# Kernel optimization log

Measured on AMD Instinct MI355X. Metric: run time of the kernel, lower is better.

Reference implementation:

```python
import math
import jax, jax.numpy as jnp
import numpy as np

C = 1024  # n_embd
B, T = 4, 2048
H = 4 * C  # mlp hidden
EPS = 1e-5


def setup_inputs() -> dict:
    key = jax.random.key(0)
    ks = jax.random.split(key, 8)
    s = 0.02
    return {
        "x": jax.random.normal(ks[0], (B, T, C), jnp.float32),
        "ln1_g": jnp.ones((C,), jnp.float32),
        "ln1_b": jnp.zeros((C,), jnp.float32),
        "w_attn": jax.random.normal(ks[1], (C, 3 * C), jnp.float32) * s,
        "b_attn": jnp.zeros((3 * C,), jnp.float32),
        "w_proj": jax.random.normal(ks[2], (C, C), jnp.float32) * s,
        "b_proj": jnp.zeros((C,), jnp.float32),
        "ln2_g": jnp.ones((C,), jnp.float32),
        "ln2_b": jnp.zeros((C,), jnp.float32),
        "w_fc": jax.random.normal(ks[3], (C, H), jnp.float32) * s,
        "b_fc": jnp.zeros((H,), jnp.float32),
        "w_mlp_proj": jax.random.normal(ks[4], (H, C), jnp.float32) * s,
        "b_mlp_proj": jnp.zeros((C,), jnp.float32),
    }


def _layernorm(x, g, b):
    mu = jnp.mean(x, axis=-1, keepdims=True)
    var = jnp.mean(jnp.square(x - mu), axis=-1, keepdims=True)
    return (x - mu) * jax.lax.rsqrt(var + EPS) * g + b


def _new_gelu(x):
    c = math.sqrt(2.0 / math.pi)
    return 0.5 * x * (1.0 + jnp.tanh(c * (x + 0.044715 * x * x * x)))


def reference(x, ln1_g, ln1_b, w_attn, b_attn, w_proj, b_proj,
              ln2_g, ln2_b, w_fc, b_fc, w_mlp_proj, b_mlp_proj):
    # --- attention sublayer (single-head, full-dim, no causal mask) ---
    h = _layernorm(x, ln1_g, ln1_b)
    qkv = h @ w_attn + b_attn              # [B,T,3C]
    q, k, v = jnp.split(qkv, 3, axis=-1)   # each [B,T,C]
    scale = 1.0 / math.sqrt(C)
    att = jnp.einsum("btc,bsc->bts", q, k) * scale  # [B,T,T]
    att = jax.nn.softmax(att, axis=-1)
    y = jnp.einsum("bts,bsc->btc", att, v)
    y = y @ w_proj + b_proj
    x = x + y
    # --- MLP sublayer ---
    h2 = _layernorm(x, ln2_g, ln2_b)
    m = _new_gelu(h2 @ w_fc + b_fc) @ w_mlp_proj + b_mlp_proj
    return x + m
```

## Files before the change

kernel.cpp:

```cpp
#include <hip/hip_runtime.h>

typedef __bf16 bf16;
typedef bf16 bf16x8 __attribute__((ext_vector_type(8)));
typedef bf16 bf16x4 __attribute__((ext_vector_type(4)));
typedef float f32x4 __attribute__((ext_vector_type(4)));

#define C_DIM 1024
#define T_DIM 2048
#define B_DIM 4
#define H_DIM 4096

__device__ inline void gld_lds16(const bf16* g, bf16* l) {
    __builtin_amdgcn_global_load_lds(
        (const __attribute__((address_space(1))) unsigned int*)g,
        (__attribute__((address_space(3))) unsigned int*)l,
        16, 0, 0);
}

__device__ inline float fast_gelu(float u) {
    float k2 = 1.5957691216057308f * u + 0.07135480895843475f * u * u * u;
    float t = __expf(-k2);
    return u * __builtin_amdgcn_rcpf(1.0f + t);
}

template <int EPI, typename OutT, int BN>
__launch_bounds__(512, 2)
__global__ void gemm8p(const bf16* __restrict__ A, int lda, long long sA,
                       const bf16* __restrict__ Bt, int ldb, long long sB,
                       OutT* __restrict__ Cout, int ldc, long long sC,
                       const float* __restrict__ bias,
                       const float* __restrict__ resid, long long sR,
                       float alpha, int K) {
    constexpr int BQ = BN / 128;
    constexpr int FM = (BN == 256) ? 8 : 4;
    constexpr int AW = (BN == 256) ? 128 : 64;

    const int z = blockIdx.z;
    A += (long long)z * sA;
    Bt += (long long)z * sB;
    Cout += (long long)z * sC;
    if (resid) resid += (long long)z * sR;

    const int rowBase = blockIdx.x * 256;
    const int colBase = blockIdx.y * BN;

    __shared__ __align__(16) bf16 As[2 * 2 * 256 * 32];
    __shared__ __align__(16) bf16 Bs[2 * 2 * BN * 32];

    const int tid = threadIdx.x;
    const int w = tid >> 6;
    const int lane = tid & 63;
    const int wm = (BN == 256) ? (w >> 2) : (w >> 1);
    const int wn = (BN == 256) ? (w & 3) : (w & 1);
    const int lr = lane & 15, lc = lane >> 4;

    const int gchunk = (tid & 3) ^ ((tid >> 3) & 3);
    const bf16* Ag = A + (size_t)(rowBase + (tid >> 2)) * lda + gchunk * 8;
    const bf16* Bg = Bt + (size_t)(colBase + (tid >> 2)) * ldb + gchunk * 8;
    const size_t ldaL = (size_t)lda, ldbL = (size_t)ldb;
    bf16* AsW = As + w * 512;
    bf16* BsW = Bs + w * 512;

    const int rchunk = lc ^ ((lr >> 1) & 3);
    const int aBase = wm * (AW * 32) + lr * 32 + rchunk * 8;
    const int bBase = wn * 2048 + lr * 32 + rchunk * 8;

#define STAGE_A(buf, ks, tau) do {                                         \
        const bf16* _g = Ag + (size_t)(tau) * 64 + (ks) * 32;              \
        bf16* _l = AsW + ((buf) * 2 + (ks)) * 8192;                        \
        gld_lds16(_g, _l);                                                 \
        gld_lds16(_g + 128 * ldaL, _l + 4096);                             \
    } while (0)

#define STAGE_B(buf, ks, tau) do {                                         \
        const bf16* _g = Bg + (size_t)(tau) * 64 + (ks) * 32;              \
        bf16* _l = BsW + ((buf) * 2 + (ks)) * (BN * 32);                   \
        gld_lds16(_g, _l);                                                 \
        if constexpr (BQ == 2) gld_lds16(_g + 128 * ldbL, _l + 4096);      \
    } while (0)

#define LOAD_A(buf, ks, rh) do {                                           \
        _Pragma("unroll")                                                  \
        for (int i = 0; i < 4; i++)                                        \
            af[i] = *(const bf16x8*)(As + aBase + ((buf) * 2 + (ks)) * 8192 \
                                     + (rh) * 2048 + i * 512);             \
    } while (0)

#define LOAD_B(dst, buf, ks) do {                                          \
        _Pragma("unroll")                                                  \
        for (int j = 0; j < 4; j++)                                        \
            dst[j] = *(const bf16x8*)(Bs + bBase + ((buf) * 2 + (ks)) * (BN * 32) \
                                      + j * 512);                          \
    } while (0)

#define MMA(rh, bfr) do {                                                  \
        __builtin_amdgcn_s_setprio(1);                                     \
        _Pragma("unroll")                                                  \
        for (int i = 0; i < 4; i++)                                        \
            _Pragma("unroll")                                              \
            for (int j = 0; j < 4; j++)                                    \
                acc[(rh) * 4 + i][j] = __builtin_amdgcn_mfma_f32_16x16x32_bf16( \
                    af[i], bfr[j], acc[(rh) * 4 + i][j], 0, 0, 0);         \
        __builtin_amdgcn_s_setprio(0);                                     \
    } while (0)

#define BAR() do { __builtin_amdgcn_s_barrier(); __builtin_amdgcn_sched_barrier(0); } while (0)
#define VMC(n) asm volatile("s_waitcnt vmcnt(" #n ")" ::: "memory")

    f32x4 acc[FM][4] = {};
    bf16x8 af[4], b0[4], b1[4];

    const int NT = K >> 6;

    if constexpr (BN == 256) {
        STAGE_B(0, 0, 0);
        STAGE_A(0, 0, 0);
        STAGE_B(0, 1, 0);
        STAGE_A(0, 1, 0);
        STAGE_B(1, 0, 1);
        STAGE_A(1, 0, 1);
        STAGE_B(1, 1, 1);
        VMC(6);
        BAR();

        for (int t = 0; t < NT; t += 2) {
            const bool more2 = (t + 2 < NT);
            LOAD_A(0, 0, 0); LOAD_B(b0, 0, 0);
            STAGE_A(1, 1, t + 1);
            BAR(); MMA(0, b0); BAR();

            LOAD_A(0, 0, 1);
            if (more2) STAGE_B(0, 0, t + 2);
            BAR(); MMA(1, b0); BAR();

            LOAD_A(0, 1, 0); LOAD_B(b1, 0, 1);
            if (more2) STAGE_A(0, 0, t + 2);
            BAR(); MMA(0, b1); BAR();

            LOAD_A(0, 1, 1);
            if (more2) STAGE_B(0, 1, t + 2);
            BAR(); MMA(1, b1);
            if (more2) VMC(6); else VMC(0);
            BAR();

            LOAD_A(1, 0, 0); LOAD_B(b0, 1, 0);
            if (more2) STAGE_A(0, 1, t + 2);
            BAR(); MMA(0, b0); BAR();

            LOAD_A(1, 0, 1);
            if (more2) STAGE_B(1, 0, t + 3);
            BAR(); MMA(1, b0); BAR();

            LOAD_A(1, 1, 0); LOAD_B(b1, 1, 1);
            if (more2) STAGE_A(1, 0, t + 3);
            BAR(); MMA(0, b1); BAR();

            LOAD_A(1, 1, 1);
            if (more2) STAGE_B(1, 1, t + 3);
            BAR(); MMA(1, b1);
            if (more2) VMC(6);
            BAR();
        }
    } else {
        STAGE_A(0, 0, 0);
        STAGE_B(0, 0, 0);
        STAGE_A(0, 1, 0);
        STAGE_B(0, 1, 0);
        STAGE_A(1, 0, 1);
        STAGE_B(1, 0, 1);
        VMC(3);
        BAR();

        for (int t = 0; t < NT; t += 2) {
            const bool more2 = (t + 2 < NT);
            LOAD_A(0, 0, 0); LOAD_B(b0, 0, 0);
            STAGE_A(1, 1, t + 1); STAGE_B(1, 1, t + 1);
            BAR(); MMA(0, b0); BAR();
            LOAD_A(0, 1, 0); LOAD_B(b1, 0, 1);
            if (more2) { STAGE_A(0, 0, t + 2); STAGE_B(0, 0, t + 2); }
            BAR(); MMA(0, b1);
            if (more2) VMC(3); else VMC(0);
            BAR();
            LOAD_A(1, 0, 0); LOAD_B(b0, 1, 0);
            if (more2) { STAGE_A(0, 1, t + 2); STAGE_B(0, 1, t + 2); }
            BAR(); MMA(0, b0); BAR();
            LOAD_A(1, 1, 0); LOAD_B(b1, 1, 1);
            if (more2) { STAGE_A(1, 0, t + 3); STAGE_B(1, 0, t + 3); }
            BAR(); MMA(0, b1);
            if (more2) VMC(3);
            BAR();
        }
    }

#undef STAGE_A
#undef STAGE_B
#undef LOAD_A
#undef LOAD_B
#undef MMA
#undef BAR
#undef VMC

    float bval[4];
#pragma unroll
    for (int j = 0; j < 4; j++)
        bval[j] = bias ? bias[colBase + wn * 64 + j * 16 + lr] : 0.0f;

#pragma unroll
    for (int fi = 0; fi < FM; fi++) {
        const int row = rowBase + wm * AW + fi * 16 + lc * 4;
#pragma unroll
        for (int fj = 0; fj < 4; fj++) {
            const int col = colBase + wn * 64 + fj * 16 + lr;
#pragma unroll
            for (int r = 0; r < 4; r++) {
                float v = acc[fi][fj][r] * alpha + bval[fj];
                if constexpr (EPI == 1) v = fast_gelu(v);
                if constexpr (EPI == 2) v += resid[(size_t)(row + r) * ldc + col];
                Cout[(size_t)(row + r) * ldc + col] = (OutT)v;
            }
        }
    }
}

__launch_bounds__(256)
__global__ void ln_kernel(const float* __restrict__ x, const float* __restrict__ g,
                          const float* __restrict__ b, bf16* __restrict__ out) {
    __shared__ float red[4];
    const int row = blockIdx.x;
    const int tid = threadIdx.x;
    const float4* xr = (const float4*)(x + (size_t)row * C_DIM);
    float4 v = xr[tid];
    float s = v.x + v.y + v.z + v.w;
#pragma unroll
    for (int m = 32; m; m >>= 1) s += __shfl_xor(s, m, 64);
    if ((tid & 63) == 0) red[tid >> 6] = s;
    __syncthreads();
    const float mu = (red[0] + red[1] + red[2] + red[3]) * (1.0f / C_DIM);
    const float dx = v.x - mu, dy = v.y - mu, dz = v.z - mu, dw = v.w - mu;
    float q = dx * dx + dy * dy + dz * dz + dw * dw;
#pragma unroll
    for (int m = 32; m; m >>= 1) q += __shfl_xor(q, m, 64);
    __syncthreads();
    if ((tid & 63) == 0) red[tid >> 6] = q;
    __syncthreads();
    const float var = (red[0] + red[1] + red[2] + red[3]) * (1.0f / C_DIM);
    const float rs = rsqrtf(var + 1e-5f);
    const float4 gg = ((const float4*)g)[tid];
    const float4 bb = ((const float4*)b)[tid];
    bf16x4 o;
    o[0] = (bf16)(dx * rs * gg.x + bb.x);
    o[1] = (bf16)(dy * rs * gg.y + bb.y);
    o[2] = (bf16)(dz * rs * gg.z + bb.z);
    o[3] = (bf16)(dw * rs * gg.w + bb.w);
    ((bf16x4*)(out + (size_t)row * C_DIM))[tid] = o;
}

__launch_bounds__(256)
__global__ void softmax_kernel(const bf16* __restrict__ S, bf16* __restrict__ P) {
    __shared__ float red[4];
    const size_t base = (size_t)blockIdx.x * T_DIM;
    const int tid = threadIdx.x;
    bf16x8 sv = ((const bf16x8*)(S + base))[tid];
    float e[8];
#pragma unroll
    for (int i = 0; i < 8; i++) e[i] = (float)sv[i];
    float mx = e[0];
#pragma unroll
    for (int i = 1; i < 8; i++) mx = fmaxf(mx, e[i]);
#pragma unroll
    for (int m = 32; m; m >>= 1) mx = fmaxf(mx, __shfl_xor(mx, m, 64));
    if ((tid & 63) == 0) red[tid >> 6] = mx;
    __syncthreads();
    mx = fmaxf(fmaxf(red[0], red[1]), fmaxf(red[2], red[3]));
    float s = 0.0f;
#pragma unroll
    for (int i = 0; i < 8; i++) {
        e[i] = __expf(e[i] - mx);
        s += e[i];
    }
#pragma unroll
    for (int m = 32; m; m >>= 1) s += __shfl_xor(s, m, 64);
    __syncthreads();
    if ((tid & 63) == 0) red[tid >> 6] = s;
    __syncthreads();
    const float inv = 1.0f / (red[0] + red[1] + red[2] + red[3]);
    bf16x8 p;
#pragma unroll
    for (int i = 0; i < 8; i++) p[i] = (bf16)(e[i] * inv);
    ((bf16x8*)(P + base))[tid] = p;
}

__global__ void transpose_f2b_all(const float* __restrict__ s0, bf16* __restrict__ d0,
                                  const float* __restrict__ s1, bf16* __restrict__ d1,
                                  const float* __restrict__ s2, bf16* __restrict__ d2,
                                  const float* __restrict__ s3, bf16* __restrict__ d3) {
    __shared__ float tile[32][33];
    int id = blockIdx.x;
    const float* src;
    bf16* dst;
    int R, Cc, local;
    if (id < 3072)       { src = s0; dst = d0; R = 1024; Cc = 3072; local = id; }
    else if (id < 4096)  { src = s1; dst = d1; R = 1024; Cc = 1024; local = id - 3072; }
    else if (id < 8192)  { src = s2; dst = d2; R = 1024; Cc = 4096; local = id - 4096; }
    else                 { src = s3; dst = d3; R = 4096; Cc = 1024; local = id - 8192; }
    const int tilesX = Cc >> 5;
    const int bx = (local % tilesX) * 32;
    const int by = (local / tilesX) * 32;
    const int tx = threadIdx.x, ty = threadIdx.y;
    for (int i = ty; i < 32; i += 8)
        tile[i][tx] = src[(size_t)(by + i) * Cc + bx + tx];
    __syncthreads();
    for (int i = ty; i < 32; i += 8)
        dst[(size_t)(bx + i) * R + by + tx] = (bf16)tile[tx][i];
}

__global__ void transpose_b2b(const bf16* __restrict__ src, int ldsrc, long long sstride,
                              bf16* __restrict__ dst, long long dstride, int R) {
    __shared__ bf16 tile[32][33];
    src += (long long)blockIdx.z * sstride;
    dst += (long long)blockIdx.z * dstride;
    const int bx = blockIdx.x * 32;
    const int by = blockIdx.y * 32;
    const int tx = threadIdx.x, ty = threadIdx.y;
    for (int i = ty; i < 32; i += 8)
        tile[i][tx] = src[(size_t)(by + i) * ldsrc + bx + tx];
    __syncthreads();
    for (int i = ty; i < 32; i += 8)
        dst[(size_t)(bx + i) * R + by + tx] = tile[tx][i];
}

extern "C" void kernel_launch(void* const* d_in, const int* in_sizes, int n_in,
                              void* d_out, int out_size, void* d_ws, size_t ws_size,
                              hipStream_t stream) {
    const float* x      = (const float*)d_in[0];
    const float* ln1_g  = (const float*)d_in[1];
    const float* ln1_b  = (const float*)d_in[2];
    const float* w_attn = (const float*)d_in[3];
    const float* b_attn = (const float*)d_in[4];
    const float* w_proj = (const float*)d_in[5];
    const float* b_proj = (const float*)d_in[6];
    const float* ln2_g  = (const float*)d_in[7];
    const float* ln2_b  = (const float*)d_in[8];
    const float* w_fc   = (const float*)d_in[9];
    const float* b_fc   = (const float*)d_in[10];
    const float* w_mlp  = (const float*)d_in[11];
    const float* b_mlp  = (const float*)d_in[12];
    float* out = (float*)d_out;

    const int M = B_DIM * T_DIM;

    char* base = (char*)d_ws;
    size_t off = 0;
    auto alloc = [&](size_t bytes) -> char* {
        char* p = base + off;
        off += (bytes + 255) & ~(size_t)255;
        return p;
    };
    bf16* wT_attn = (bf16*)alloc((size_t)3072 * 1024 * 2);
    bf16* wT_proj = (bf16*)alloc((size_t)1024 * 1024 * 2);
    bf16* wT_fc   = (bf16*)alloc((size_t)4096 * 1024 * 2);
    bf16* wT_mlp  = (bf16*)alloc((size_t)1024 * 4096 * 2);
    bf16* h       = (bf16*)alloc((size_t)M * 1024 * 2);
    bf16* qkv     = (bf16*)alloc((size_t)M * 3072 * 2);
    bf16* vT      = (bf16*)alloc((size_t)B_DIM * 1024 * 2048 * 2);
    bf16* S       = (bf16*)alloc((size_t)B_DIM * 2048 * 2048 * 2);
    bf16* P       = (bf16*)alloc((size_t)B_DIM * 2048 * 2048 * 2);
    bf16* y       = (bf16*)alloc((size_t)M * 1024 * 2);
    float* x2     = (float*)alloc((size_t)M * 1024 * 4);
    bf16* act     = (bf16*)S;

    const dim3 tb(32, 8);

    transpose_f2b_all<<<12288, tb, 0, stream>>>(w_attn, wT_attn, w_proj, wT_proj,
                                                w_fc, wT_fc, w_mlp, wT_mlp);

    ln_kernel<<<M, 256, 0, stream>>>(x, ln1_g, ln1_b, h);

    gemm8p<0, bf16, 128><<<dim3(32, 24, 1), 512, 0, stream>>>(
        h, 1024, 0, wT_attn, 1024, 0, qkv, 3072, 0, b_attn, nullptr, 0, 1.0f, 1024);

    transpose_b2b<<<dim3(1024 / 32, 2048 / 32, B_DIM), tb, 0, stream>>>(
        qkv + 2 * C_DIM, 3072, (long long)T_DIM * 3072, vT, (long long)C_DIM * T_DIM, T_DIM);

    gemm8p<0, bf16, 256><<<dim3(8, 8, B_DIM), 512, 0, stream>>>(
        qkv, 3072, (long long)T_DIM * 3072,
        qkv + C_DIM, 3072, (long long)T_DIM * 3072,
        S, 2048, (long long)T_DIM * T_DIM, nullptr, nullptr, 0, 0.03125f, 1024);

    softmax_kernel<<<B_DIM * T_DIM, 256, 0, stream>>>(S, P);

    gemm8p<0, bf16, 128><<<dim3(8, 8, B_DIM), 512, 0, stream>>>(
        P, 2048, (long long)T_DIM * T_DIM,
        vT, 2048, (long long)C_DIM * T_DIM,
        y, 1024, (long long)T_DIM * C_DIM, nullptr, nullptr, 0, 1.0f, 2048);

    gemm8p<2, float, 128><<<dim3(32, 8, 1), 512, 0, stream>>>(
        y, 1024, 0, wT_proj, 1024, 0, x2, 1024, 0, b_proj, x, 0, 1.0f, 1024);

    ln_kernel<<<M, 256, 0, stream>>>(x2, ln2_g, ln2_b, h);

    gemm8p<1, bf16, 256><<<dim3(32, 16, 1), 512, 0, stream>>>(
        h, 1024, 0, wT_fc, 1024, 0, act, 4096, 0, b_fc, nullptr, 0, 1.0f, 1024);

    gemm8p<2, float, 128><<<dim3(32, 8, 1), 512, 0, stream>>>(
        act, 4096, 0, wT_mlp, 4096, 0, out, 1024, 0, b_mlp, x2, 0, 1.0f, 4096);
}
```

Before: 516.2 us.

## Swizzle workgroup order, peel last GEMM iteration, relax waitcnt and scheduling barriers

Remaps the block index so consecutive workgroups are spread across 8 groups (XCD-aware tile ordering), to improve L2 locality across the chiplets. The main K loop is restructured to always prefetch, with a peeled final iteration, finer-grained vmcnt waits that allow more loads in flight, and sched_barrier removed from BAR so the compiler can interleave instructions more freely. Loosening the waits risks races if the vmcnt counts do not match the issued loads, and dropping the scheduling fences may let the compiler reorder in unintended ways.

```diff
diff --git a/kernel.cpp b/kernel.cpp
--- a/kernel.cpp
+++ b/kernel.cpp
@@ -41,8 +41,12 @@
     Cout += (long long)z * sC;
     if (resid) resid += (long long)z * sR;
 
-    const int rowBase = blockIdx.x * 256;
-    const int colBase = blockIdx.y * BN;
+    const int gx = gridDim.x;
+    const int nwg = gx * gridDim.y;
+    int bid = blockIdx.y * gx + blockIdx.x;
+    bid = (bid & 7) * (nwg >> 3) + (bid >> 3);
+    const int rowBase = (bid % gx) * 256;
+    const int colBase = (bid / gx) * BN;
 
     __shared__ __align__(16) bf16 As[2 * 2 * 256 * 32];
     __shared__ __align__(16) bf16 Bs[2 * 2 * BN * 32];
@@ -104,7 +108,7 @@
         __builtin_amdgcn_s_setprio(0);                                     \
     } while (0)
 
-#define BAR() do { __builtin_amdgcn_s_barrier(); __builtin_amdgcn_sched_barrier(0); } while (0)
+#define BAR() __builtin_amdgcn_s_barrier()
 #define VMC(n) asm volatile("s_waitcnt vmcnt(" #n ")" ::: "memory")
 
     f32x4 acc[FM][4] = {};
@@ -120,46 +124,61 @@
         STAGE_B(1, 0, 1);
         STAGE_A(1, 0, 1);
         STAGE_B(1, 1, 1);
-        VMC(6);
         BAR();
 
-        for (int t = 0; t < NT; t += 2) {
-            const bool more2 = (t + 2 < NT);
+        for (int t = 0; t < NT - 2; t += 2) {
+            VMC(10);
             LOAD_A(0, 0, 0); LOAD_B(b0, 0, 0);
             STAGE_A(1, 1, t + 1);
             BAR(); MMA(0, b0); BAR();
-
             LOAD_A(0, 0, 1);
-            if (more2) STAGE_B(0, 0, t + 2);
+            STAGE_B(0, 0, t + 2);
             BAR(); MMA(1, b0); BAR();
-
+            VMC(10);
             LOAD_A(0, 1, 0); LOAD_B(b1, 0, 1);
-            if (more2) STAGE_A(0, 0, t + 2);
-            BAR(); MMA(0, b1); BAR();
-
+            STAGE_A(0, 0, t + 2);
+            BAR(); MMA(0, b1); BAR();
             LOAD_A(0, 1, 1);
-            if (more2) STAGE_B(0, 1, t + 2);
-            BAR(); MMA(1, b1);
-            if (more2) VMC(6); else VMC(0);
-            BAR();
-
+            STAGE_B(0, 1, t + 2);
+            BAR(); MMA(1, b1); BAR();
+            VMC(10);
             LOAD_A(1, 0, 0); LOAD_B(b0, 1, 0);
-            if (more2) STAGE_A(0, 1, t + 2);
-            BAR(); MMA(0, b0); BAR();
-
+            STAGE_A(0, 1, t + 2);
+            BAR(); MMA(0, b0); BAR();
             LOAD_A(1, 0, 1);
-            if (more2) STAGE_B(1, 0, t + 3);
+            STAGE_B(1, 0, t + 3);
             BAR(); MMA(1, b0); BAR();
-
+            VMC(10);
             LOAD_A(1, 1, 0); LOAD_B(b1, 1, 1);
-            if (more2) STAGE_A(1, 0, t + 3);
-            BAR(); MMA(0, b1); BAR();
-
+            STAGE_A(1, 0, t + 3);
+            BAR(); MMA(0, b1); BAR();
             LOAD_A(1, 1, 1);
-            if (more2) STAGE_B(1, 1, t + 3);
-            BAR(); MMA(1, b1);
-            if (more2) VMC(6);
-            BAR();
+            STAGE_B(1, 1, t + 3);
+            BAR(); MMA(1, b1); BAR();
+        }
+        {
+            const int t = NT - 2;
+            VMC(10);
+            LOAD_A(0, 0, 0); LOAD_B(b0, 0, 0);
+            STAGE_A(1, 1, t + 1);
+            BAR(); MMA(0, b0); BAR();
+            LOAD_A(0, 0, 1);
+            BAR(); MMA(1, b0); BAR();
+            VMC(8);
+            LOAD_A(0, 1, 0); LOAD_B(b1, 0, 1);
+            BAR(); MMA(0, b1); BAR();
+            LOAD_A(0, 1, 1);
+            BAR(); MMA(1, b1); BAR();
+            VMC(4);
+            LOAD_A(1, 0, 0); LOAD_B(b0, 1, 0);
+            BAR(); MMA(0, b0); BAR();
+            LOAD_A(1, 0, 1);
+            BAR(); MMA(1, b0); BAR();
+            VMC(0);
+            LOAD_A(1, 1, 0); LOAD_B(b1, 1, 1);
+            BAR(); MMA(0, b1); BAR();
+            LOAD_A(1, 1, 1);
+            MMA(1, b1);
         }
     } else {
         STAGE_A(0, 0, 0);
@@ -168,27 +187,41 @@
         STAGE_B(0, 1, 0);
         STAGE_A(1, 0, 1);
         STAGE_B(1, 0, 1);
-        VMC(3);
         BAR();
 
-        for (int t = 0; t < NT; t += 2) {
-            const bool more2 = (t + 2 < NT);
+        for (int t = 0; t < NT - 2; t += 2) {
+            VMC(6);
             LOAD_A(0, 0, 0); LOAD_B(b0, 0, 0);
             STAGE_A(1, 1, t + 1); STAGE_B(1, 1, t + 1);
             BAR(); MMA(0, b0); BAR();
+            VMC(6);
             LOAD_A(0, 1, 0); LOAD_B(b1, 0, 1);
-            if (more2) { STAGE_A(0, 0, t + 2); STAGE_B(0, 0, t + 2); }
-            BAR(); MMA(0, b1);
-            if (more2) VMC(3); else VMC(0);
-            BAR();
+            STAGE_A(0, 0, t + 2); STAGE_B(0, 0, t + 2);
+            BAR(); MMA(0, b1); BAR();
+            VMC(6);
             LOAD_A(1, 0, 0); LOAD_B(b0, 1, 0);
-            if (more2) { STAGE_A(0, 1, t + 2); STAGE_B(0, 1, t + 2); }
-            BAR(); MMA(0, b0); BAR();
+            STAGE_A(0, 1, t + 2); STAGE_B(0, 1, t + 2);
+            BAR(); MMA(0, b0); BAR();
+            VMC(6);
             LOAD_A(1, 1, 0); LOAD_B(b1, 1, 1);
-            if (more2) { STAGE_A(1, 0, t + 3); STAGE_B(1, 0, t + 3); }
-            BAR(); MMA(0, b1);
-            if (more2) VMC(3);
-            BAR();
+            STAGE_A(1, 0, t + 3); STAGE_B(1, 0, t + 3);
+            BAR(); MMA(0, b1); BAR();
+        }
+        {
+            const int t = NT - 2;
+            VMC(6);
+            LOAD_A(0, 0, 0); LOAD_B(b0, 0, 0);
+            STAGE_A(1, 1, t + 1); STAGE_B(1, 1, t + 1);
+            BAR(); MMA(0, b0); BAR();
+            VMC(6);
+            LOAD_A(0, 1, 0); LOAD_B(b1, 0, 1);
+            BAR(); MMA(0, b1); BAR();
+            VMC(3);
+            LOAD_A(1, 0, 0); LOAD_B(b0, 1, 0);
+            BAR(); MMA(0, b0); BAR();
+            VMC(0);
+            LOAD_A(1, 1, 0); LOAD_B(b1, 1, 1);
+            MMA(0, b1);
         }
     }
 
```

New measurement: 553.3 us. 7.2% more time.

## Unify GEMM main loop into single per-k-slice pipeline with peeled epilogue

Applied to the files above, without the earlier changes.

Replaces the two BN-specialised main loops, which split each k-slice into row halves with separate A-fragment loads and MMAs, with one schedule. Each k-slice now loads all FM A-fragments and the B fragments at once and issues the full MMA block, with the vmcnt waits moved ahead of the LDS reads and a peeled tail for the last two tiles. It also drops the sched_barrier from BAR. The aim is fewer barriers and better MFMA batching, at the cost of more live fragment registers (af[FM]) and a risk that the changed vmcnt counts cause incorrect waits or lower occupancy.

```diff
diff --git a/kernel.cpp b/kernel.cpp
--- a/kernel.cpp
+++ b/kernel.cpp
@@ -79,126 +79,100 @@
         if constexpr (BQ == 2) gld_lds16(_g + 128 * ldbL, _l + 4096);      \
     } while (0)
 
-#define LOAD_A(buf, ks, rh) do {                                           \
+#define LOAD_AF(buf, ks) do {                                              \
         _Pragma("unroll")                                                  \
-        for (int i = 0; i < 4; i++)                                        \
+        for (int i = 0; i < FM; i++)                                       \
             af[i] = *(const bf16x8*)(As + aBase + ((buf) * 2 + (ks)) * 8192 \
-                                     + (rh) * 2048 + i * 512);             \
-    } while (0)
-
-#define LOAD_B(dst, buf, ks) do {                                          \
+                                     + i * 512);                           \
+    } while (0)
+
+#define LOAD_BF(buf, ks) do {                                              \
         _Pragma("unroll")                                                  \
         for (int j = 0; j < 4; j++)                                        \
-            dst[j] = *(const bf16x8*)(Bs + bBase + ((buf) * 2 + (ks)) * (BN * 32) \
+            bfv[j] = *(const bf16x8*)(Bs + bBase + ((buf) * 2 + (ks)) * (BN * 32) \
                                       + j * 512);                          \
     } while (0)
 
-#define MMA(rh, bfr) do {                                                  \
+#define MMAALL() do {                                                      \
         __builtin_amdgcn_s_setprio(1);                                     \
         _Pragma("unroll")                                                  \
-        for (int i = 0; i < 4; i++)                                        \
+        for (int i = 0; i < FM; i++)                                       \
             _Pragma("unroll")                                              \
             for (int j = 0; j < 4; j++)                                    \
-                acc[(rh) * 4 + i][j] = __builtin_amdgcn_mfma_f32_16x16x32_bf16( \
-                    af[i], bfr[j], acc[(rh) * 4 + i][j], 0, 0, 0);         \
+                acc[i][j] = __builtin_amdgcn_mfma_f32_16x16x32_bf16(       \
+                    af[i], bfv[j], acc[i][j], 0, 0, 0);                    \
         __builtin_amdgcn_s_setprio(0);                                     \
     } while (0)
 
-#define BAR() do { __builtin_amdgcn_s_barrier(); __builtin_amdgcn_sched_barrier(0); } while (0)
-#define VMC(n) asm volatile("s_waitcnt vmcnt(" #n ")" ::: "memory")
+#define BAR() __builtin_amdgcn_s_barrier()
+#define VMCS() do {                                                        \
+        if constexpr (BN == 256) asm volatile("s_waitcnt vmcnt(8)" ::: "memory"); \
+        else                     asm volatile("s_waitcnt vmcnt(6)" ::: "memory"); \
+    } while (0)
+#define VMCH() do {                                                        \
+        if constexpr (BN == 256) asm volatile("s_waitcnt vmcnt(4)" ::: "memory"); \
+        else                     asm volatile("s_waitcnt vmcnt(3)" ::: "memory"); \
+    } while (0)
+#define VMC0() asm volatile("s_waitcnt vmcnt(0)" ::: "memory")
 
     f32x4 acc[FM][4] = {};
-    bf16x8 af[4], b0[4], b1[4];
+    bf16x8 af[FM], bfv[4];
 
     const int NT = K >> 6;
 
-    if constexpr (BN == 256) {
-        STAGE_B(0, 0, 0);
-        STAGE_A(0, 0, 0);
-        STAGE_B(0, 1, 0);
-        STAGE_A(0, 1, 0);
-        STAGE_B(1, 0, 1);
-        STAGE_A(1, 0, 1);
-        STAGE_B(1, 1, 1);
-        VMC(6);
-        BAR();
-
-        for (int t = 0; t < NT; t += 2) {
-            const bool more2 = (t + 2 < NT);
-            LOAD_A(0, 0, 0); LOAD_B(b0, 0, 0);
-            STAGE_A(1, 1, t + 1);
-            BAR(); MMA(0, b0); BAR();
-
-            LOAD_A(0, 0, 1);
-            if (more2) STAGE_B(0, 0, t + 2);
-            BAR(); MMA(1, b0); BAR();
-
-            LOAD_A(0, 1, 0); LOAD_B(b1, 0, 1);
-            if (more2) STAGE_A(0, 0, t + 2);
-            BAR(); MMA(0, b1); BAR();
-
-            LOAD_A(0, 1, 1);
-            if (more2) STAGE_B(0, 1, t + 2);
-            BAR(); MMA(1, b1);
-            if (more2) VMC(6); else VMC(0);
-            BAR();
-
-            LOAD_A(1, 0, 0); LOAD_B(b0, 1, 0);
-            if (more2) STAGE_A(0, 1, t + 2);
-            BAR(); MMA(0, b0); BAR();
-
-            LOAD_A(1, 0, 1);
-            if (more2) STAGE_B(1, 0, t + 3);
-            BAR(); MMA(1, b0); BAR();
-
-            LOAD_A(1, 1, 0); LOAD_B(b1, 1, 1);
-            if (more2) STAGE_A(1, 0, t + 3);
-            BAR(); MMA(0, b1); BAR();
-
-            LOAD_A(1, 1, 1);
-            if (more2) STAGE_B(1, 1, t + 3);
-            BAR(); MMA(1, b1);
-            if (more2) VMC(6);
-            BAR();
-        }
-    } else {
-        STAGE_A(0, 0, 0);
-        STAGE_B(0, 0, 0);
-        STAGE_A(0, 1, 0);
-        STAGE_B(0, 1, 0);
-        STAGE_A(1, 0, 1);
-        STAGE_B(1, 0, 1);
-        VMC(3);
-        BAR();
-
-        for (int t = 0; t < NT; t += 2) {
-            const bool more2 = (t + 2 < NT);
-            LOAD_A(0, 0, 0); LOAD_B(b0, 0, 0);
-            STAGE_A(1, 1, t + 1); STAGE_B(1, 1, t + 1);
-            BAR(); MMA(0, b0); BAR();
-            LOAD_A(0, 1, 0); LOAD_B(b1, 0, 1);
-            if (more2) { STAGE_A(0, 0, t + 2); STAGE_B(0, 0, t + 2); }
-            BAR(); MMA(0, b1);
-            if (more2) VMC(3); else VMC(0);
-            BAR();
-            LOAD_A(1, 0, 0); LOAD_B(b0, 1, 0);
-            if (more2) { STAGE_A(0, 1, t + 2); STAGE_B(0, 1, t + 2); }
-            BAR(); MMA(0, b0); BAR();
-            LOAD_A(1, 1, 0); LOAD_B(b1, 1, 1);
-            if (more2) { STAGE_A(1, 0, t + 3); STAGE_B(1, 0, t + 3); }
-            BAR(); MMA(0, b1);
-            if (more2) VMC(3);
-            BAR();
-        }
+    STAGE_A(0, 0, 0); STAGE_B(0, 0, 0);
+    STAGE_A(0, 1, 0); STAGE_B(0, 1, 0);
+    STAGE_A(1, 0, 1); STAGE_B(1, 0, 1);
+    BAR();
+
+    for (int t = 0; t < NT - 2; t += 2) {
+        VMCS();
+        LOAD_AF(0, 0); LOAD_BF(0, 0);
+        STAGE_A(1, 1, t + 1); STAGE_B(1, 1, t + 1);
+        BAR(); MMAALL(); BAR();
+
+        VMCS();
+        LOAD_AF(0, 1); LOAD_BF(0, 1);
+        STAGE_A(0, 0, t + 2); STAGE_B(0, 0, t + 2);
+        BAR(); MMAALL(); BAR();
+
+        VMCS();
+        LOAD_AF(1, 0); LOAD_BF(1, 0);
+        STAGE_A(0, 1, t + 2); STAGE_B(0, 1, t + 2);
+        BAR(); MMAALL(); BAR();
+
+        VMCS();
+        LOAD_AF(1, 1); LOAD_BF(1, 1);
+        STAGE_A(1, 0, t + 3); STAGE_B(1, 0, t + 3);
+        BAR(); MMAALL(); BAR();
     }
+
+    VMCS();
+    LOAD_AF(0, 0); LOAD_BF(0, 0);
+    STAGE_A(1, 1, NT - 1); STAGE_B(1, 1, NT - 1);
+    BAR(); MMAALL(); BAR();
+
+    VMCS();
+    LOAD_AF(0, 1); LOAD_BF(0, 1);
+    BAR(); MMAALL(); BAR();
+
+    VMCH();
+    LOAD_AF(1, 0); LOAD_BF(1, 0);
+    BAR(); MMAALL(); BAR();
+
+    VMC0();
+    LOAD_AF(1, 1); LOAD_BF(1, 1);
+    MMAALL();
 
 #undef STAGE_A
 #undef STAGE_B
-#undef LOAD_A
-#undef LOAD_B
-#undef MMA
+#undef LOAD_AF
+#undef LOAD_BF
+#undef MMAALL
 #undef BAR
-#undef VMC
+#undef VMCS
+#undef VMCH
+#undef VMC0
 
     float bval[4];
 #pragma unroll
```

Result: no change. 519.0 us (+0.5%).
